# Optimization experiments

Hardware: AMD Instinct MI355X
Metric: run time of the kernel (lower is better)

Reference implementation:

```python
import jax, jax.numpy as jnp
import numpy as np

B, N, D_PATCH = 32, 196, 768
TKN, QK, H, HID = 768, 64, 12, 3072
K_STEPS = 12
ALPHA = 1.0
BETA = 1.0 / (QK ** 0.5)
EPS = 1e-5


def setup_inputs() -> dict:
    key = jax.random.key(0)
    ks = jax.random.split(key, 8)
    w_std = 0.002
    return {
        "x": jax.random.normal(ks[0], (B, N, D_PATCH), jnp.float32),
        "w_enc": jax.random.normal(ks[1], (TKN, D_PATCH), jnp.float32) * 0.02,
        "b_enc": jnp.zeros((TKN,), jnp.float32),
        "cls_tok": jnp.ones((1, 1, TKN), jnp.float32),
        "pos": jax.random.normal(ks[2], (1, N + 1, TKN), jnp.float32) * w_std,
        "eln_gamma": jnp.ones((1,), jnp.float32),
        "eln_bias": jnp.zeros((TKN,), jnp.float32),
        "wq": jax.random.normal(ks[3], (H, QK, TKN), jnp.float32) * w_std,
        "wk": jax.random.normal(ks[4], (H, QK, TKN), jnp.float32) * w_std,
        "w_hop": jax.random.normal(ks[5], (HID, TKN), jnp.float32) * 0.02,
        "dec_ln_w": jnp.ones((TKN,), jnp.float32),
        "dec_ln_b": jnp.zeros((TKN,), jnp.float32),
        "w_dec": jax.random.normal(ks[6], (D_PATCH, TKN), jnp.float32) * 0.02,
        "b_dec": jnp.zeros((D_PATCH,), jnp.float32),
    }


def _energy(g, wq, wk, w_hop):
    # attention energy: non-softmax, -1/beta * sum logsumexp(beta * A)
    q = jnp.einsum('bnd,hzd->bnhz', g, wq)
    k = jnp.einsum('bnd,hzd->bnhz', g, wk)
    A = jnp.einsum('bqhz,bkhz->bhqk', q, k)  # [B,H,N+1,N+1]
    e_attn = (-1.0 / BETA) * jnp.sum(jax.nn.logsumexp(BETA * A, axis=-1))
    # Hopfield energy: -0.5 * sum relu(g W^T)^2
    h = jnp.einsum('bnd,fd->bnf', g, w_hop)  # [B,N+1,HID]
    e_hop = -0.5 * jnp.sum(jax.nn.relu(h) ** 2)
    return e_attn + e_hop


def _energy_ln(x, gamma, bias):
    xm = x - x.mean(-1, keepdims=True)
    o = xm / jnp.sqrt((xm ** 2).mean(-1, keepdims=True) + EPS)
    return gamma * o + bias


def _layernorm(x, w, b):
    mu = x.mean(-1, keepdims=True)
    xm = x - mu
    var = (xm ** 2).mean(-1, keepdims=True)
    return xm / jnp.sqrt(var + EPS) * w + b


def reference(x, w_enc, b_enc, cls_tok, pos, eln_gamma, eln_bias,
              wq, wk, w_hop, dec_ln_w, dec_ln_b, w_dec, b_dec):
    # encode: Linear(d_patch -> tkn)
    t = jnp.einsum('bnd,td->bnt', x, w_enc) + b_enc
    # prepend cls, add positional encoding
    cls = jnp.broadcast_to(cls_tok, (t.shape[0], 1, TKN))
    t = jnp.concatenate([cls, t], axis=1) + pos  # [B, N+1, TKN]

    grad_e = jax.grad(lambda g: _energy(g, wq, wk, w_hop))
    for _ in range(K_STEPS):  # fixed unroll over time steps (single block)
        g = _energy_ln(t, eln_gamma, eln_bias)
        t = t - ALPHA * grad_e(g)

    # decode: LayerNorm + Linear(tkn -> d_patch)
    y = _layernorm(t, dec_ln_w, dec_ln_b)
    y = jnp.einsum('bnt,dt->bnd', y, w_dec) + b_dec
    return y[:, 1:]  # drop cls token (use_cls=False)
```

## Files before the change

### kernel.cpp

```cpp
#include <hip/hip_runtime.h>
#include <hip/hip_bf16.h>

typedef __hip_bfloat16 bf16;
typedef short s8 __attribute__((ext_vector_type(8)));
typedef short sv4 __attribute__((ext_vector_type(4)));
typedef float f4 __attribute__((ext_vector_type(4)));

#define BETA 0.125f
#define EPS 1e-5f

__device__ __forceinline__ void gld16(const void* g, void* l){
    __builtin_amdgcn_global_load_lds(
        (const __attribute__((address_space(1))) void*)g,
        (__attribute__((address_space(3))) void*)l, 16, 0, 0);
}

__global__ __launch_bounds__(256) void pre_k(
    const float* __restrict__ wq, const float* __restrict__ wk, const float* __restrict__ w_hop,
    const float* __restrict__ w_enc, const float* __restrict__ w_dec,
    const float* __restrict__ x, const float* __restrict__ cls, const float* __restrict__ pos,
    bf16* __restrict__ B1, bf16* __restrict__ we_, bf16* __restrict__ wd_,
    bf16* __restrict__ g_, float* __restrict__ t_)
{
    long e = (long)blockIdx.x*256 + threadIdx.x;
    if (e < 3538944L){
        float v;
        if (e < 589824L)        v = wq[e];
        else if (e < 1179648L)  v = wk[e - 589824L];
        else                    v = w_hop[e - 1179648L];
        B1[e] = __float2bfloat16(v);
    } else if (e < 4128768L){
        long i = e - 3538944L;  we_[i] = __float2bfloat16(w_enc[i]);
    } else if (e < 4718592L){
        long i = e - 4128768L;  wd_[i] = __float2bfloat16(w_dec[i]);
    } else if (e < 9633792L){
        long i = e - 4718592L;
        long row = i / 768;
        g_[i] = (row < 6272) ? __float2bfloat16(x[i]) : __float2bfloat16(0.f);
    } else {
        long i = e - 9633792L;
        int b = (int)(i / 768), c = (int)(i % 768);
        if (b < 32) t_[((long)b*197)*768 + c] = cls[c] + pos[c];
    }
}

__global__ __launch_bounds__(256) void tr_k(const short* __restrict__ Bi, short* __restrict__ Bo){
    __shared__ short t[32][33];
    int i0 = blockIdx.x*32, j0 = blockIdx.y*32;
    int li = threadIdx.x & 31, lj = threadIdx.x >> 5;
    #pragma unroll
    for (int r=0;r<4;r++) t[lj+8*r][li] = Bi[(long)(i0+lj+8*r)*768 + j0+li];
    __syncthreads();
    #pragma unroll
    for (int r=0;r<4;r++) Bo[(long)(j0+lj+8*r)*4608 + i0+li] = t[li][lj+8*r];
}

template<int MODE>
__global__ __launch_bounds__(256) void big_gemm(
    const short* __restrict__ A, int lda,
    const short* __restrict__ B, int ldb,
    float* __restrict__ Cf, bf16* __restrict__ Cb, int ldc,
    int K, int Nn, int Nm, int relu0, long zoff,
    const float* __restrict__ bias, const float* __restrict__ pos)
{
    const int f = blockIdx.x;
    const int npg = 16*Nn;
    const int grp = f / npg;
    const int first_m = grp*16;
    const int gs = (Nm - first_m < 16) ? (Nm - first_m) : 16;
    const int rem = f % npg;
    const int bm = first_m + rem % gs;
    const int bn = rem / gs;

    __shared__ short lsA[8192];
    __shared__ short lsB[8192];
    const int tid = threadIdx.x;
    const int w = tid>>6, l = tid&63;
    const int m0 = bm*128, n0 = bn*128;
    const int srow = tid>>2;
    const int qglob = ((tid&3) - (tid>>3)) & 3;
    const int scol = qglob*8;
    int koff, Ks;
    if (MODE==1){ Ks = K>>1; koff = blockIdx.z * Ks; Cf += (size_t)blockIdx.z * zoff; }
    else        { Ks = K;    koff = 0; }
    const short* pa = A + (size_t)(m0+srow)*lda + koff + scol;
    const short* pb = B + (size_t)(n0+srow)*ldb + koff + scol;
    short* laP = lsA + w*512;
    short* lbP = lsB + w*512;
    const int wm = (w>>1)*64, wn = (w&1)*64;
    const int fr = l&15, fq = ((l>>4) + (fr>>1) & 3)*8;
    f4 acc[4][4] = {};
    const int nk = Ks>>6;
    for (int kt=0; kt<nk; kt++){
        const size_t ko = (size_t)kt*64;
        const size_t ra = 64*(size_t)lda, rb = 64*(size_t)ldb;
        gld16(pa + ko,           laP);
        gld16(pa + ko + ra,      laP + 2048);
        gld16(pa + ko + 32,      laP + 4096);
        gld16(pa + ko + 32 + ra, laP + 6144);
        gld16(pb + ko,           lbP);
        gld16(pb + ko + rb,      lbP + 2048);
        gld16(pb + ko + 32,      lbP + 4096);
        gld16(pb + ko + 32 + rb, lbP + 6144);
        __syncthreads();
        #pragma unroll
        for (int ks=0; ks<2; ks++){
            s8 af[4], bfr[4];
            #pragma unroll
            for (int i=0;i<4;i++) af[i]  = *(const s8*)(lsA + ks*4096 + (wm+i*16+fr)*32 + fq);
            #pragma unroll
            for (int j=0;j<4;j++) bfr[j] = *(const s8*)(lsB + ks*4096 + (wn+j*16+fr)*32 + fq);
            #pragma unroll
            for (int i=0;i<4;i++)
                #pragma unroll
                for (int j=0;j<4;j++)
                    acc[i][j] = __builtin_amdgcn_mfma_f32_16x16x32_bf16(af[i], bfr[j], acc[i][j], 0,0,0);
        }
        __syncthreads();
    }
    const int er = (l>>4)*4;
    const int ec = l&15;
    #pragma unroll
    for (int i=0;i<4;i++){
        #pragma unroll
        for (int j=0;j<4;j++){
            int gr0 = m0 + wm + i*16 + er;
            int gc  = n0 + wn + j*16 + ec;
            #pragma unroll
            for (int r=0;r<4;r++){
                float v = acc[i][j][r];
                int gr = gr0 + r;
                if (MODE==0){
                    if (gc >= relu0) v = v>0.f ? v : 0.f;
                    Cb[(size_t)gr*ldc + gc] = __float2bfloat16(v);
                } else if (MODE==1){
                    Cf[(size_t)gr*ldc + gc] = v;
                } else if (MODE==2){
                    if (gr < 6272){
                        int b = gr/196, n = gr%196;
                        Cf[((size_t)b*197 + n + 1)*768 + gc] = v + bias[gc] + pos[(long)(n+1)*768+gc];
                    }
                } else {
                    if (gr < 6272) Cf[(size_t)gr*ldc + gc] = v + bias[gc];
                }
            }
        }
    }
}

template<int MODE>
__global__ __launch_bounds__(256, 2) void wide_gemm(
    const short* __restrict__ A, int lda,
    const short* __restrict__ B, int ldb,
    float* __restrict__ Cf, float* __restrict__ Cf2,
    bf16* __restrict__ Cb, int ldc,
    int K, int Nn, int Nm, int relu0, long zoff)
{
    const int f = blockIdx.x;
    const int npg = 16*Nn;
    const int grp = f / npg;
    const int first_m = grp*16;
    const int gs = (Nm - first_m < 16) ? (Nm - first_m) : 16;
    const int rem = f % npg;
    const int bm = first_m + rem % gs;
    const int bn = rem / gs;

    __shared__ short lsA[16384];
    __shared__ short lsB[8192];
    const int tid = threadIdx.x;
    const int w = tid>>6, l = tid&63;
    const int m0 = bm*256, n0 = bn*128;

    int Ks, koff; float* Cp = Cf;
    if (MODE==1){ Ks = K/3; koff = blockIdx.z * Ks;
                  Cp = (blockIdx.z==2) ? Cf2 : Cf + (size_t)blockIdx.z * zoff; }
    else        { Ks = K; koff = 0; }
    const int NT = Ks>>6;

    const short* sA[4]; const short* sB[2];
    #pragma unroll
    for (int j=0;j<4;j++){
        int c = j*256 + tid;
        int r = (c>>2)&255, qd = c&3;
        int qs = (qd - (r>>1)) & 3;
        sA[j] = A + (size_t)(m0+r)*lda + koff + qs*8;
    }
    #pragma unroll
    for (int j=0;j<2;j++){
        int c = j*256 + tid;
        int r = (c>>2)&127, qd = c&3;
        int qs = (qd - (r>>1)) & 3;
        sB[j] = B + (size_t)(n0+r)*ldb + koff + qs*8;
    }

    const int wm = (w>>1)*128, wn = (w&1)*64;
    const int fr = l&15;
    const int fq = (((l>>4) + (fr>>1)) & 3)*8;
    f4 acc[8][4] = {};

    for (int kt=0; kt<NT; kt++){
        const size_t ko = (size_t)kt*64;
        short* dA = lsA + w*512;
        short* dB = lsB + w*512;
        #pragma unroll
        for (int j=0;j<4;j++){
            gld16(sA[j]+ko,      dA + j*2048);
            gld16(sA[j]+ko+32,   dA + (j+4)*2048);
        }
        #pragma unroll
        for (int j=0;j<2;j++){
            gld16(sB[j]+ko,      dB + j*2048);
            gld16(sB[j]+ko+32,   dB + (j+2)*2048);
        }
        __syncthreads();
        #pragma unroll
        for (int ks=0; ks<2; ks++){
            s8 af[8], bfr[4];
            #pragma unroll
            for (int i=0;i<8;i++) af[i]  = *(const s8*)(lsA + ks*8192 + (wm+i*16+fr)*32 + fq);
            #pragma unroll
            for (int j=0;j<4;j++) bfr[j] = *(const s8*)(lsB + ks*4096 + (wn+j*16+fr)*32 + fq);
            #pragma unroll
            for (int i=0;i<8;i++)
                #pragma unroll
                for (int j=0;j<4;j++)
                    acc[i][j] = __builtin_amdgcn_mfma_f32_16x16x32_bf16(af[i], bfr[j], acc[i][j], 0,0,0);
        }
        __syncthreads();
    }

    const int er = (l>>4)*4;
    const int ec = l&15;
    #pragma unroll
    for (int i=0;i<8;i++){
        #pragma unroll
        for (int j=0;j<4;j++){
            int gr0 = m0 + wm + i*16 + er;
            int gc  = n0 + wn + j*16 + ec;
            #pragma unroll
            for (int r=0;r<4;r++){
                float v = acc[i][j][r];
                int gr = gr0 + r;
                if (MODE==0){
                    if (gc >= relu0) v = v>0.f ? v : 0.f;
                    Cb[(size_t)gr*ldc + gc] = __float2bfloat16(v);
                } else {
                    Cp[(size_t)gr*ldc + gc] = v;
                }
            }
        }
    }
}

__global__ __launch_bounds__(256) void pack_k(const short* __restrict__ qkh,
                                              short* __restrict__ qT, short* __restrict__ kT){
    __shared__ short tq[64][65];
    __shared__ short tk[64][65];
    const int bh = blockIdx.x, b = bh/12, h = bh%12;
    const int mc = blockIdx.y*64;
    const int tid = threadIdx.x;
    #pragma unroll
    for (int e=0;e<16;e++){
        int i = tid + e*256; int r = i>>6, c = i&63;
        int mg = mc + r;
        short vq = 0, vk = 0;
        if (mg < 197){
            size_t base = (size_t)(b*197+mg)*4608 + h*64 + c;
            vq = qkh[base]; vk = qkh[base+768];
        }
        tq[r][c] = vq; tk[r][c] = vk;
    }
    __syncthreads();
    #pragma unroll
    for (int e=0;e<16;e++){
        int i = tid + e*256; int zr = i>>6, cm = i&63;
        size_t o = (size_t)bh*16384 + (size_t)zr*256 + mc + cm;
        qT[o] = tq[cm][zr];
        kT[o] = tk[cm][zr];
    }
}

__global__ __launch_bounds__(256) void attn_k(
    short* __restrict__ qkh, const short* __restrict__ qT, const short* __restrict__ kT)
{
    __shared__ short Pl[64*232];
    __shared__ short Ptl[208*72];
    const int bh = blockIdx.x, b = bh/12, h = bh%12;
    const int tid = threadIdx.x, w = tid>>6, l = tid&63;
    const int lr = l&15, lq = l>>4;
    const size_t qcol = (size_t)h*64, kcol = 768 + qcol;
    const size_t rbase = (size_t)b*197*4608;
    const short* qTp = qT + (size_t)bh*16384;
    const short* kTp = kT + (size_t)bh*16384;

    for (int i=tid; i<64*16; i+=256){ int r=i>>4, c=208+(i&15); Pl[r*232+c]=0; }

    f4 ak[13];
    #pragma unroll
    for (int t=0;t<13;t++) ak[t] = (f4){0.f,0.f,0.f,0.f};

    for (int iter=0; iter<4; iter++){
        const int m0 = iter*64;
        f4 S[13];
        #pragma unroll
        for (int t=0;t<13;t++) S[t] = (f4){0.f,0.f,0.f,0.f};
        const int mrow = m0 + w*16 + lr;
        #pragma unroll
        for (int ks=0; ks<2; ks++){
            s8 af = *(const s8*)(qkh + rbase + (size_t)mrow*4608 + qcol + ks*32 + lq*8);
            #pragma unroll
            for (int t=0;t<13;t++){
                s8 bf = *(const s8*)(qkh + rbase + (size_t)(t*16+lr)*4608 + kcol + ks*32 + lq*8);
                S[t] = __builtin_amdgcn_mfma_f32_16x16x32_bf16(af, bf, S[t], 0,0,0);
            }
        }
        __syncthreads();
        const int mbase = w*16 + lq*4;
        #pragma unroll
        for (int r=0;r<4;r++){
            float mx = -1e30f;
            #pragma unroll
            for (int t=0;t<13;t++){
                float v = S[t][r]*BETA;
                if (t==12 && lr>=5) v = -1e30f;
                S[t][r] = v;
                mx = fmaxf(mx, v);
            }
            mx = fmaxf(mx, __shfl_xor(mx,1,64)); mx = fmaxf(mx, __shfl_xor(mx,2,64));
            mx = fmaxf(mx, __shfl_xor(mx,4,64)); mx = fmaxf(mx, __shfl_xor(mx,8,64));
            float sm = 0.f;
            #pragma unroll
            for (int t=0;t<13;t++){ float e = __expf(S[t][r]-mx); S[t][r]=e; sm+=e; }
            sm += __shfl_xor(sm,1,64); sm += __shfl_xor(sm,2,64);
            sm += __shfl_xor(sm,4,64); sm += __shfl_xor(sm,8,64);
            float inv = 1.f/sm;
            bool valid = (m0 + mbase + r) < 197;
            #pragma unroll
            for (int t=0;t<13;t++) S[t][r] = valid ? S[t][r]*inv : 0.f;
        }
        #pragma unroll
        for (int t=0;t<13;t++){
            int c = t*16 + lr;
            short pb[4];
            #pragma unroll
            for (int r=0;r<4;r++){
                bf16 bv = __float2bfloat16(S[t][r]);
                pb[r] = *(short*)&bv;
                Pl[(mbase+r)*232 + c] = pb[r];
            }
            *(sv4*)(Ptl + c*72 + mbase) = (sv4){pb[0],pb[1],pb[2],pb[3]};
        }
        __syncthreads();
        f4 aq[4];
        #pragma unroll
        for (int t=0;t<4;t++) aq[t] = (f4){0.f,0.f,0.f,0.f};
        #pragma unroll
        for (int ks=0; ks<7; ks++){
            s8 af = *(const s8*)(kTp + (w*16+lr)*256 + ks*32 + lq*8);
            #pragma unroll
            for (int mt=0;mt<4;mt++){
                s8 bf = *(const s8*)(Pl + (mt*16+lr)*232 + ks*32 + lq*8);
                aq[mt] = __builtin_amdgcn_mfma_f32_16x16x32_bf16(af, bf, aq[mt], 0,0,0);
            }
        }
        #pragma unroll
        for (int mt=0;mt<4;mt++){
            int mg = m0 + mt*16 + lr;
            if (mg < 197){
                sv4 pv;
                #pragma unroll
                for (int r=0;r<4;r++){ bf16 bv=__float2bfloat16(aq[mt][r]); pv[r]=*(short*)&bv; }
                *(sv4*)(qkh + rbase + (size_t)mg*4608 + qcol + w*16 + lq*4) = pv;
            }
        }
        #pragma unroll
        for (int ks=0; ks<2; ks++){
            s8 bf = *(const s8*)(qTp + (w*16+lr)*256 + m0 + ks*32 + lq*8);
            #pragma unroll
            for (int t=0;t<13;t++){
                s8 af = *(const s8*)(Ptl + (t*16+lr)*72 + ks*32 + lq*8);
                ak[t] = __builtin_amdgcn_mfma_f32_16x16x32_bf16(af, bf, ak[t], 0,0,0);
            }
        }
    }
    #pragma unroll
    for (int t=0;t<13;t++){
        #pragma unroll
        for (int r=0;r<4;r++){
            int n = t*16 + lq*4 + r;
            if (n < 197)
                *(bf16*)(qkh + rbase + (size_t)n*4608 + kcol + w*16 + lr) = __float2bfloat16(ak[t][r]);
        }
    }
}

__global__ __launch_bounds__(256) void ln_k(
    float* __restrict__ in, bf16* __restrict__ out,
    const float* __restrict__ p0, const float* __restrict__ p1, const float* __restrict__ p2,
    const float* __restrict__ scale, const float* __restrict__ bias,
    int scalar_scale, int rowmap, int addp, int writet)
{
    int r = blockIdx.x;
    long src = rowmap ? ((long)(r/196)*197 + r%196 + 1) : (long)r;
    float* xr = in + src*768;
    int tid = threadIdx.x;
    float v0 = xr[tid], v1 = xr[tid+256], v2 = xr[tid+512];
    if (addp){
        const float* a = p0 + src*768;
        const float* b = p1 + src*768;
        const float* c = p2 + src*768;
        v0 += a[tid]     + b[tid]     + c[tid];
        v1 += a[tid+256] + b[tid+256] + c[tid+256];
        v2 += a[tid+512] + b[tid+512] + c[tid+512];
        if (writet){ xr[tid]=v0; xr[tid+256]=v1; xr[tid+512]=v2; }
    }
    __shared__ float red[4];
    float s = v0+v1+v2;
    #pragma unroll
    for (int o=1;o<64;o<<=1) s += __shfl_xor(s, o, 64);
    if ((tid&63)==0) red[tid>>6] = s;
    __syncthreads();
    float mu = (red[0]+red[1]+red[2]+red[3]) * (1.f/768.f);
    float d0=v0-mu, d1=v1-mu, d2=v2-mu;
    float q = d0*d0 + d1*d1 + d2*d2;
    #pragma unroll
    for (int o=1;o<64;o<<=1) q += __shfl_xor(q, o, 64);
    __syncthreads();
    if ((tid&63)==0) red[tid>>6] = q;
    __syncthreads();
    float ms = (red[0]+red[1]+red[2]+red[3]) * (1.f/768.f);
    float inv = rsqrtf(ms + EPS);
    bf16* o_ = out + (long)r*768;
    float s0 = scalar_scale ? scale[0] : scale[tid];
    float s1 = scalar_scale ? s0 : scale[tid+256];
    float s2 = scalar_scale ? s0 : scale[tid+512];
    o_[tid]     = __float2bfloat16(d0*inv*s0 + bias[tid]);
    o_[tid+256] = __float2bfloat16(d1*inv*s1 + bias[tid+256]);
    o_[tid+512] = __float2bfloat16(d2*inv*s2 + bias[tid+512]);
}

extern "C" void kernel_launch(void* const* d_in, const int* in_sizes, int n_in,
                              void* d_out, int out_size, void* d_ws, size_t ws_size,
                              hipStream_t stream) {
    const float* x       = (const float*)d_in[0];
    const float* w_enc   = (const float*)d_in[1];
    const float* b_enc   = (const float*)d_in[2];
    const float* cls_tok = (const float*)d_in[3];
    const float* pos     = (const float*)d_in[4];
    const float* eln_g   = (const float*)d_in[5];
    const float* eln_b   = (const float*)d_in[6];
    const float* wq      = (const float*)d_in[7];
    const float* wk      = (const float*)d_in[8];
    const float* w_hop   = (const float*)d_in[9];
    const float* dln_w   = (const float*)d_in[10];
    const float* dln_b   = (const float*)d_in[11];
    const float* w_dec   = (const float*)d_in[12];
    const float* b_dec   = (const float*)d_in[13];
    float* out = (float*)d_out;

    float* t_  = (float*)d_ws;
    bf16* g_   = (bf16*)(t_ + 6400L*768);
    bf16* qkh  = g_ + 6400L*768;
    bf16* qT   = qkh + 6400L*4608;
    bf16* kT   = qT + 384L*16384;
    float* p0  = (float*)(kT + 384L*16384);
    float* p1  = p0 + 6400L*768;
    bf16* B1   = (bf16*)(p1 + 6400L*768);
    bf16* B2   = B1 + 4608L*768;
    bf16* we_  = B2 + 768L*4608;
    bf16* wd_  = we_ + 768L*768;
    float* p2  = (float*)qT;

    dim3 blk(256);
    const long ZOFF = 6400L*768;

    pre_k<<<dim3(37728), blk, 0, stream>>>(wq, wk, w_hop, w_enc, w_dec, x, cls_tok, pos,
                                           B1, we_, wd_, g_, t_);
    tr_k<<<dim3(144,24), blk, 0, stream>>>((const short*)B1, (short*)B2);

    big_gemm<2><<<dim3(300), blk, 0, stream>>>((const short*)g_, 768, (const short*)we_, 768,
                                               t_, nullptr, 768, 768, 6, 50, 0, 0, b_enc, pos);

    for (int step=0; step<12; step++){
        ln_k<<<dim3(6304), blk, 0, stream>>>(t_, g_, p0, p1, p2, eln_g, eln_b, 1, 0, step>0, 1);
        wide_gemm<0><<<dim3(900), blk, 0, stream>>>((const short*)g_, 768, (const short*)B1, 768,
                                                    nullptr, nullptr, qkh, 4608, 768, 36, 25, 1536, 0);
        pack_k<<<dim3(384,4), blk, 0, stream>>>((const short*)qkh, (short*)qT, (short*)kT);
        attn_k<<<dim3(384), blk, 0, stream>>>((short*)qkh, (const short*)qT, (const short*)kT);
        wide_gemm<1><<<dim3(150,1,3), blk, 0, stream>>>((const short*)qkh, 4608, (const short*)B2, 4608,
                                                        p0, p2, nullptr, 768, 4608, 6, 25, 0, ZOFF);
    }

    ln_k<<<dim3(6272), blk, 0, stream>>>(t_, g_, p0, p1, p2, dln_w, dln_b, 0, 1, 1, 0);
    big_gemm<3><<<dim3(300), blk, 0, stream>>>((const short*)g_, 768, (const short*)wd_, 768,
                                               out, nullptr, 768, 768, 6, 50, 0, 0, b_dec, nullptr);
}
```

Before: 2.392 ms.

## Fuse Q/K transpose packing into the QKH GEMM epilogue

```diff
diff --git a/kernel.cpp b/kernel.cpp
--- a/kernel.cpp
+++ b/kernel.cpp
@@ -5,6 +5,7 @@
 typedef short s8 __attribute__((ext_vector_type(8)));
 typedef short sv4 __attribute__((ext_vector_type(4)));
 typedef float f4 __attribute__((ext_vector_type(4)));
+typedef int i4 __attribute__((ext_vector_type(4)));
 
 #define BETA 0.125f
 #define EPS 1e-5f
@@ -42,6 +43,18 @@
         int b = (int)(i / 768), c = (int)(i % 768);
         if (b < 32) t_[((long)b*197)*768 + c] = cls[c] + pos[c];
     }
+}
+
+__global__ __launch_bounds__(256) void zqt_k(i4* __restrict__ p){
+    p[(long)blockIdx.x*256 + threadIdx.x] = (i4){0,0,0,0};
+}
+
+__global__ __launch_bounds__(256) void zpad_k(i4* __restrict__ qt){
+    int t = blockIdx.x*256 + threadIdx.x;
+    int arr = t / 196608;
+    int u = t - arr*196608;
+    int bhz = u >> 3, slot = u & 7;
+    qt[(long)arr*786432 + (long)bhz*32 + 24 + slot] = (i4){0,0,0,0};
 }
 
 __global__ __launch_bounds__(256) void tr_k(const short* __restrict__ Bi, short* __restrict__ Bo){
@@ -231,8 +244,20 @@
 
     const int er = (l>>4)*4;
     const int ec = l&15;
+    const bool doTr = (MODE==0) && (bn < 12);
+    short* qTs = (short*)Cf;
+    short* kTs = (short*)Cf2;
     #pragma unroll
     for (int i=0;i<8;i++){
+        int bArr[4], mgArr[4];
+        if (doTr){
+            #pragma unroll
+            for (int r=0;r<4;r++){
+                int gr = m0 + wm + i*16 + er + r;
+                int bb = gr/197;
+                bArr[r] = bb; mgArr[r] = gr - bb*197;
+            }
+        }
         #pragma unroll
         for (int j=0;j<4;j++){
             int gr0 = m0 + wm + i*16 + er;
@@ -243,40 +268,20 @@
                 int gr = gr0 + r;
                 if (MODE==0){
                     if (gc >= relu0) v = v>0.f ? v : 0.f;
-                    Cb[(size_t)gr*ldc + gc] = __float2bfloat16(v);
+                    bf16 bv = __float2bfloat16(v);
+                    Cb[(size_t)gr*ldc + gc] = bv;
+                    if (doTr && gr < 6304){
+                        int qk = (gc < 768) ? gc : gc - 768;
+                        short* base = (gc < 768) ? qTs : kTs;
+                        int h = qk>>6, z = qk&63;
+                        base[((size_t)(bArr[r]*12 + h))*16384 + (size_t)z*256 + mgArr[r]]
+                            = *(short*)&bv;
+                    }
                 } else {
                     Cp[(size_t)gr*ldc + gc] = v;
                 }
             }
         }
-    }
-}
-
-__global__ __launch_bounds__(256) void pack_k(const short* __restrict__ qkh,
-                                              short* __restrict__ qT, short* __restrict__ kT){
-    __shared__ short tq[64][65];
-    __shared__ short tk[64][65];
-    const int bh = blockIdx.x, b = bh/12, h = bh%12;
-    const int mc = blockIdx.y*64;
-    const int tid = threadIdx.x;
-    #pragma unroll
-    for (int e=0;e<16;e++){
-        int i = tid + e*256; int r = i>>6, c = i&63;
-        int mg = mc + r;
-        short vq = 0, vk = 0;
-        if (mg < 197){
-            size_t base = (size_t)(b*197+mg)*4608 + h*64 + c;
-            vq = qkh[base]; vk = qkh[base+768];
-        }
-        tq[r][c] = vq; tk[r][c] = vk;
-    }
-    __syncthreads();
-    #pragma unroll
-    for (int e=0;e<16;e++){
-        int i = tid + e*256; int zr = i>>6, cm = i&63;
-        size_t o = (size_t)bh*16384 + (size_t)zr*256 + mc + cm;
-        qT[o] = tq[cm][zr];
-        kT[o] = tk[cm][zr];
     }
 }
 
@@ -476,6 +481,7 @@
 
     pre_k<<<dim3(37728), blk, 0, stream>>>(wq, wk, w_hop, w_enc, w_dec, x, cls_tok, pos,
                                            B1, we_, wd_, g_, t_);
+    zqt_k<<<dim3(6144), blk, 0, stream>>>((i4*)qT);
     tr_k<<<dim3(144,24), blk, 0, stream>>>((const short*)B1, (short*)B2);
 
     big_gemm<2><<<dim3(300), blk, 0, stream>>>((const short*)g_, 768, (const short*)we_, 768,
@@ -483,9 +489,9 @@
 
     for (int step=0; step<12; step++){
         ln_k<<<dim3(6304), blk, 0, stream>>>(t_, g_, p0, p1, p2, eln_g, eln_b, 1, 0, step>0, 1);
+        zpad_k<<<dim3(1536), blk, 0, stream>>>((i4*)qT);
         wide_gemm<0><<<dim3(900), blk, 0, stream>>>((const short*)g_, 768, (const short*)B1, 768,
-                                                    nullptr, nullptr, qkh, 4608, 768, 36, 25, 1536, 0);
-        pack_k<<<dim3(384,4), blk, 0, stream>>>((const short*)qkh, (short*)qT, (short*)kT);
+                                                    (float*)qT, (float*)kT, qkh, 4608, 768, 36, 25, 1536, 0);
         attn_k<<<dim3(384), blk, 0, stream>>>((short*)qkh, (const short*)qT, (const short*)kT);
         wide_gemm<1><<<dim3(150,1,3), blk, 0, stream>>>((const short*)qkh, 4608, (const short*)B2, 4608,
                                                         p0, p2, nullptr, 768, 4608, 6, 25, 0, ZOFF);
```

Result: slower. 2.689 ms (+12.4%).
